# Kernel optimization log

Measured on AMD Instinct MI355X. Metric: run time of the kernel, lower is better.

Reference implementation:

```python
import jax, jax.numpy as jnp
import numpy as np

B, N, DIM, H, DH = 8, 1024, 512, 8, 64
INNER = H * DH  # 512
G = DH // 4     # SE(3) groups of size 4 per head


def setup_inputs() -> dict:
    key = jax.random.key(0)
    ks = jax.random.split(key, 6)
    x = jax.random.normal(ks[0], (B, N, DIM), jnp.float32)
    rotations = jax.random.normal(ks[1], (B, N, 3, 3), jnp.float32)
    translations = jax.random.normal(ks[2], (B, N, 3), jnp.float32)
    # JaxLinear init: trunc-normal std = 1/sqrt(fan_in), zero bias
    w_qkv = jax.random.normal(ks[3], (DIM, 3 * INNER), jnp.float32) * (1.0 / np.sqrt(DIM))
    b_qkv = jnp.zeros((3 * INNER,), jnp.float32)
    w_out = jax.random.normal(ks[4], (INNER, DIM), jnp.float32) * (1.0 / np.sqrt(INNER))
    b_out = jnp.zeros((DIM,), jnp.float32)
    return {"x": x, "rotations": rotations, "translations": translations,
            "w_qkv": w_qkv, "b_qkv": b_qkv, "w_out": w_out, "b_out": b_out}


def _apply_pose(P, t, transpose):
    # P: [B,N,4,4]; t: [B,H,N,DH] -> reshape to groups of 4 and rotate each group
    tg = t.reshape(B, H, N, G, 4)
    sub = 'bnji,bhncj->bhnci' if transpose else 'bnij,bhncj->bhnci'
    return jnp.einsum(sub, P, tg).reshape(B, H, N, DH)


def reference(x, rotations, translations, w_qkv, b_qkv, w_out, b_out):
    scale = DH ** -0.5
    qkv = x @ w_qkv + b_qkv                      # [B,N,3*INNER]
    q, k, v = jnp.split(qkv, 3, axis=-1)
    to_heads = lambda t: t.reshape(B, N, H, DH).transpose(0, 2, 1, 3)  # b n (h d) -> b h n d
    q, k, v = to_heads(q), to_heads(k), to_heads(v)

    # SE(3) pose matrices
    eye4 = jnp.eye(4, dtype=x.dtype)
    Rt = jnp.swapaxes(rotations, -1, -2)
    t_inv = -jnp.einsum('bnij,bnj->bni', Rt, translations)
    P_qinv = (jnp.broadcast_to(eye4, (B, N, 4, 4))
              .at[..., :3, :3].set(Rt)
              .at[..., :3, 3].set(t_inv))       # inverted query poses
    P_kv = (jnp.broadcast_to(eye4, (B, N, 4, 4))
            .at[..., :3, :3].set(rotations)
            .at[..., :3, 3].set(translations))  # key/value poses

    # per-token rotation of q/k/v (q uses P_qinv^T per original einsum)
    q = _apply_pose(P_qinv, q, transpose=True)
    k = _apply_pose(P_kv, k, transpose=False)
    v = _apply_pose(P_kv, v, transpose=False)   # v_transform=True

    attn = jax.nn.softmax(jnp.einsum('bhqd,bhkd->bhqk', q, k) * scale, axis=-1)
    out = jnp.einsum('bhqk,bhkd->bhqd', attn, v)
    out = _apply_pose(P_qinv, out, transpose=False)  # inverse transform on output

    out = out.transpose(0, 2, 1, 3).reshape(B, N, INNER)  # b h n d -> b n (h d)
    return out @ w_out + b_out
```

## Files before the change

kernel.cpp:

```cpp
#include <hip/hip_runtime.h>
#include <math.h>

#define BSZ   8
#define NSEQ  1024
#define DIM   512
#define NH    8
#define DH    64
#define INNER 512
#define NTOK  (BSZ*NSEQ)
#define QKVN  (3*INNER)

typedef __bf16 bf16x8 __attribute__((ext_vector_type(8)));
typedef float  f32x4  __attribute__((ext_vector_type(4)));

#define QSCL (0.125f * 1.44269504088896f)

#define ATTN_P_OFF 49152
#define ATTN_LDS   67584

static __device__ __forceinline__ ushort f2bf(float f) {
    union { float f; unsigned u; } v; v.f = f;
    unsigned r = (v.u + 0x7FFFu + ((v.u >> 16) & 1u)) >> 16;
    return (ushort)r;
}
static __device__ __forceinline__ float bf2f(ushort u) {
    union { unsigned u; float f; } v; v.u = ((unsigned)u) << 16;
    return v.f;
}
static __device__ __forceinline__ void split2(float x, ushort& h, ushort& l) {
    h = f2bf(x);
    l = f2bf(x - bf2f(h));
}
static __device__ __forceinline__ void async16(const void* g, void* l) {
    __builtin_amdgcn_global_load_lds(
        (const __attribute__((address_space(1))) unsigned int*)g,
        (__attribute__((address_space(3))) unsigned int*)l, 16, 0, 0);
}

__global__ __launch_bounds__(256) void split_cvt_kernel(
    const float* __restrict__ in, ushort* __restrict__ oh, ushort* __restrict__ ol)
{
    const int i = blockIdx.x * 256 + threadIdx.x;
    float4 v = ((const float4*)in)[i];
    ushort4 h, l;
    split2(v.x, h.x, l.x); split2(v.y, h.y, l.y);
    split2(v.z, h.z, l.z); split2(v.w, h.w, l.w);
    ((ushort4*)oh)[i] = h;
    ((ushort4*)ol)[i] = l;
}

__global__ __launch_bounds__(256) void tconv_kernel(
    const float* __restrict__ in, ushort* __restrict__ outh, int K, int F)
{
    __shared__ float tile[32][33];
    const int bx = blockIdx.x;
    const int by = blockIdx.y;
    const int lx = threadIdx.x & 31, ly = threadIdx.x >> 5;
#pragma unroll
    for (int u = 0; u < 4; u++) {
        const int k = by*32 + ly + u*8;
        tile[ly + u*8][lx] = in[(size_t)k*F + bx*32 + lx];
    }
    __syncthreads();
#pragma unroll
    for (int u = 0; u < 4; u++) {
        const int f = bx*32 + ly + u*8;
        outh[(size_t)f*K + by*32 + lx] = f2bf(tile[lx][ly + u*8]);
    }
}

__global__ __launch_bounds__(256) void qkv_gemm_split(
    const ushort* __restrict__ Agh, const ushort* __restrict__ Bgh,
    const ushort* __restrict__ Bgl,
    const float* __restrict__ bias, const float* __restrict__ rot,
    const float* __restrict__ trans,
    ushort* __restrict__ qb, ushort* __restrict__ kb, ushort* __restrict__ vt)
{
    extern __shared__ __align__(16) char smem[];

    const int tid  = threadIdx.x;
    const int lane = tid & 63;
    const int w    = tid >> 6;
    const int c    = lane & 15;
    const int quad = lane >> 4;
    const int wr   = w >> 1, wc = w & 1;
    const int tn   = blockIdx.x;
    const int tf   = blockIdx.y;

    f32x4 acc[4][4] = {};

    const ushort* wp = (w == 0) ? Agh : (w == 1) ? Bgh : Bgl;
    const ushort* wbase = wp + (size_t)((w == 0 ? tf : tn)*128 + c)*DIM + quad*8;
    const int lbase = w * 8192;

    auto stage = [&](int k0, int buf) {
        if (w < 3) {
#pragma unroll
            for (int g = 0; g < 8; g++)
                async16(wbase + (size_t)g*16*DIM + k0,
                        smem + buf*24576 + lbase + g*1024);
        }
    };

    stage(0, 0);

    for (int ch = 0; ch < 16; ch++) {
        const int cur = ch & 1, nxt = cur ^ 1;
        if (ch < 15) {
            stage((ch+1)*32, nxt);
            __asm__ volatile("s_waitcnt vmcnt(8)\n\ts_barrier" ::: "memory");
        } else {
            __asm__ volatile("s_waitcnt vmcnt(0)\n\ts_barrier" ::: "memory");
        }

        const char* B = smem + cur*24576;
        bf16x8 fa[4], fbh[4], fbl[4];
#pragma unroll
        for (int i = 0; i < 4; i++)
            fa[i] = *(const bf16x8*)(B + (wr*4 + i)*1024 + lane*16);
#pragma unroll
        for (int j = 0; j < 4; j++) {
            fbh[j] = *(const bf16x8*)(B +  8192 + (wc*4 + j)*1024 + lane*16);
            fbl[j] = *(const bf16x8*)(B + 16384 + (wc*4 + j)*1024 + lane*16);
        }
#pragma unroll
        for (int i = 0; i < 4; i++)
#pragma unroll
            for (int j = 0; j < 4; j++) {
                acc[i][j] = __builtin_amdgcn_mfma_f32_16x16x32_bf16(
                    fa[i], fbh[j], acc[i][j], 0, 0, 0);
                acc[i][j] = __builtin_amdgcn_mfma_f32_16x16x32_bf16(
                    fa[i], fbl[j], acc[i][j], 0, 0, 0);
            }
        __asm__ volatile("s_waitcnt lgkmcnt(0)\n\ts_barrier" ::: "memory");
    }

    const int sec = tf >> 2;

#pragma unroll
    for (int j = 0; j < 4; j++) {
        const int tc = tn*128 + wc*64 + j*16 + c;
        const int bb = tc >> 10, n = tc & 1023;
        const float* R = rot   + (size_t)(bb*NSEQ + n)*9;
        const float* T = trans + (size_t)(bb*NSEQ + n)*3;
        const float R0=R[0],R1=R[1],R2=R[2],R3=R[3],R4=R[4],R5=R[5],R6=R[6],R7=R[7],R8=R[8];
        const float T0=T[0],T1=T[1],T2=T[2];
        float ti0 = 0.f, ti1 = 0.f, ti2 = 0.f;
        if (sec == 0) {
            ti0 = -(R0*T0 + R3*T1 + R6*T2);
            ti1 = -(R1*T0 + R4*T1 + R7*T2);
            ti2 = -(R2*T0 + R5*T1 + R8*T2);
        }
#pragma unroll
        for (int i = 0; i < 4; i++) {
            const int fr = tf*128 + wr*64 + i*16 + quad*4;
            const int fl = fr & 511;
            const int h  = fl >> 6, d = fl & 63;
            float4 bv = *(const float4*)(bias + fr);
            const float g0 = acc[i][j][0] + bv.x;
            const float g1 = acc[i][j][1] + bv.y;
            const float g2 = acc[i][j][2] + bv.z;
            const float g3 = acc[i][j][3] + bv.w;
            if (sec == 0) {
                float o0 = (R0*g0 + R1*g1 + R2*g2) * QSCL;
                float o1 = (R3*g0 + R4*g1 + R5*g2) * QSCL;
                float o2 = (R6*g0 + R7*g1 + R8*g2) * QSCL;
                float o3 = (ti0*g0 + ti1*g1 + ti2*g2 + g3) * QSCL;
                ushort4 ov = { f2bf(o0), f2bf(o1), f2bf(o2), f2bf(o3) };
                *(ushort4*)(qb + ((size_t)((bb*NH + h)*NSEQ + n))*DH + d) = ov;
            } else {
                float o0 = R0*g0 + R1*g1 + R2*g2 + T0*g3;
                float o1 = R3*g0 + R4*g1 + R5*g2 + T1*g3;
                float o2 = R6*g0 + R7*g1 + R8*g2 + T2*g3;
                float o3 = g3;
                if (sec == 1) {
                    ushort4 ov = { f2bf(o0), f2bf(o1), f2bf(o2), f2bf(o3) };
                    *(ushort4*)(kb + ((size_t)((bb*NH + h)*NSEQ + n))*DH + d) = ov;
                } else {
                    ushort* vtb = vt + ((size_t)(bb*NH + h)*DH + d)*NSEQ + n;
                    vtb[0*NSEQ] = f2bf(o0);
                    vtb[1*NSEQ] = f2bf(o1);
                    vtb[2*NSEQ] = f2bf(o2);
                    vtb[3*NSEQ] = f2bf(o3);
                }
            }
        }
    }
}

__global__ __launch_bounds__(256) void attn_mfma_kernel(
    const ushort* __restrict__ qb, const ushort* __restrict__ kb,
    const ushort* __restrict__ vt, const float* __restrict__ rot,
    const float* __restrict__ trans, ushort* __restrict__ om)
{
    extern __shared__ __align__(16) char smem[];

    const int tid  = threadIdx.x;
    const int lane = tid & 63;
    const int w    = tid >> 6;
    const int c    = lane & 15;
    const int quad = lane >> 4;

    const int qt = blockIdx.x;
    const int bh = blockIdx.y;
    const int bb = bh >> 3, h = bh & 7;

    const ushort* Q = qb + (size_t)bh * NSEQ * DH;
    const ushort* K = kb + (size_t)bh * NSEQ * DH;
    const ushort* V = vt + (size_t)bh * DH * NSEQ;

    bf16x8 qf[2][2];
#pragma unroll
    for (int m = 0; m < 2; m++) {
        const ushort* qrow = Q + (size_t)(qt*128 + w*32 + m*16 + c)*DH + quad*8;
        qf[m][0] = *(const bf16x8*)(qrow);
        qf[m][1] = *(const bf16x8*)(qrow + 32);
    }

    f32x4 Oacc[2][4] = {};
    float lsum[2][4] = {};

    auto stage = [&](int kt, int buf) {
#pragma unroll
        for (int u = 0; u < 2; u++) {
            const int seg = w + u*4;
            const int nt = seg >> 1, hh = seg & 1;
            const ushort* g = K + (size_t)(kt*64 + nt*16 + c)*DH + hh*32 + quad*8;
            async16(g, smem + buf*16384 + seg*1024);
        }
#pragma unroll
        for (int u = 0; u < 2; u++) {
            const int s2 = w + u*4;
            const int nt = s2 >> 1, kc = s2 & 1;
            const ushort* g = V + (size_t)(nt*16 + c)*NSEQ + kt*64 + kc*32 + quad*8;
            async16(g, smem + buf*16384 + 8192 + s2*1024);
        }
    };

    stage(0, 0);
    stage(1, 1);

    for (int kt = 0; kt < 16; kt++) {
        const int cur = kt % 3;
        if (kt < 15) {
            __asm__ volatile("s_waitcnt vmcnt(4)\n\ts_barrier" ::: "memory");
        } else {
            __asm__ volatile("s_waitcnt vmcnt(0)\n\ts_barrier" ::: "memory");
        }
        if (kt < 14) stage(kt + 2, (kt + 2) % 3);

        const char* Kb = smem + cur*16384;
        const char* Vb = smem + cur*16384 + 8192;

        f32x4 s[2][4];
#pragma unroll
        for (int nt = 0; nt < 4; nt++) {
            bf16x8 k0 = *(const bf16x8*)(Kb + (nt*2+0)*1024 + lane*16);
            bf16x8 k1 = *(const bf16x8*)(Kb + (nt*2+1)*1024 + lane*16);
#pragma unroll
            for (int m = 0; m < 2; m++) {
                f32x4 a = {0.f, 0.f, 0.f, 0.f};
                a = __builtin_amdgcn_mfma_f32_16x16x32_bf16(qf[m][0], k0, a, 0, 0, 0);
                a = __builtin_amdgcn_mfma_f32_16x16x32_bf16(qf[m][1], k1, a, 0, 0, 0);
                s[m][nt] = a;
            }
        }

#pragma unroll
        for (int m = 0; m < 2; m++) {
            ushort (*Psw)[72] = (ushort (*)[72])(smem + ATTN_P_OFF + (w*2+m)*2304);
#pragma unroll
            for (int nt = 0; nt < 4; nt++)
#pragma unroll
                for (int r = 0; r < 4; r++) {
                    const float p = exp2f(s[m][nt][r]);
                    lsum[m][r] += p;
                    Psw[quad*4 + r][nt*16 + c] = (ushort)__builtin_bit_cast(
                        unsigned short, (__bf16)p);
                }
        }
        __asm__ volatile("s_waitcnt lgkmcnt(0)" ::: "memory");

#pragma unroll
        for (int kc = 0; kc < 2; kc++) {
            bf16x8 vfr[4];
#pragma unroll
            for (int nt = 0; nt < 4; nt++)
                vfr[nt] = *(const bf16x8*)(Vb + (nt*2+kc)*1024 + lane*16);
#pragma unroll
            for (int m = 0; m < 2; m++) {
                ushort (*Psw)[72] = (ushort (*)[72])(smem + ATTN_P_OFF + (w*2+m)*2304);
                bf16x8 a = *(const bf16x8*)&Psw[c][kc*32 + quad*8];
#pragma unroll
                for (int nt = 0; nt < 4; nt++)
                    Oacc[m][nt] = __builtin_amdgcn_mfma_f32_16x16x32_bf16(
                        a, vfr[nt], Oacc[m][nt], 0, 0, 0);
            }
        }
    }

#pragma unroll
    for (int mk = 1; mk < 16; mk <<= 1)
#pragma unroll
        for (int m = 0; m < 2; m++)
#pragma unroll
            for (int r = 0; r < 4; r++)
                lsum[m][r] += __shfl_xor(lsum[m][r], mk);

    __syncthreads();
    float (*Osh)[68] = (float (*)[68])smem;
    {
        float inv[2][4];
#pragma unroll
        for (int m = 0; m < 2; m++)
#pragma unroll
            for (int r = 0; r < 4; r++) inv[m][r] = 1.f / lsum[m][r];
#pragma unroll
        for (int m = 0; m < 2; m++)
#pragma unroll
            for (int nt = 0; nt < 4; nt++)
#pragma unroll
                for (int r = 0; r < 4; r++)
                    Osh[w*32 + m*16 + quad*4 + r][nt*16 + c] =
                        Oacc[m][nt][r] * inv[m][r];
    }
    __syncthreads();

#pragma unroll
    for (int u = 0; u < 8; u++) {
        const int t   = tid + u*256;
        const int row = t >> 4;
        const int g   = t & 15;
        const int n   = qt*128 + row;
        const float o0 = Osh[row][g*4+0], o1 = Osh[row][g*4+1];
        const float o2 = Osh[row][g*4+2], o3 = Osh[row][g*4+3];
        const float* R = rot   + (size_t)(bb*NSEQ + n)*9;
        const float* T = trans + (size_t)(bb*NSEQ + n)*3;
        const float ti0 = -(R[0]*T[0] + R[3]*T[1] + R[6]*T[2]);
        const float ti1 = -(R[1]*T[0] + R[4]*T[1] + R[7]*T[2]);
        const float ti2 = -(R[2]*T[0] + R[5]*T[1] + R[8]*T[2]);
        const float p0 = R[0]*o0 + R[3]*o1 + R[6]*o2 + ti0*o3;
        const float p1 = R[1]*o0 + R[4]*o1 + R[7]*o2 + ti1*o3;
        const float p2 = R[2]*o0 + R[5]*o1 + R[8]*o2 + ti2*o3;
        const float p3 = o3;
        ushort4 hv = { f2bf(p0), f2bf(p1), f2bf(p2), f2bf(p3) };
        *(ushort4*)(om + (size_t)(bb*NSEQ + n)*INNER + h*DH + g*4) = hv;
    }
}

__global__ __launch_bounds__(256) void out_gemm_mfma(
    const ushort* __restrict__ Ag, const ushort* __restrict__ Bg,
    const float* __restrict__ bias, float* __restrict__ out)
{
    extern __shared__ __align__(16) char smem[];

    const int tid  = threadIdx.x;
    const int lane = tid & 63;
    const int w    = tid >> 6;
    const int c    = lane & 15;
    const int quad = lane >> 4;
    const int wr   = w >> 1, wc = w & 1;
    const int tn   = blockIdx.x;
    const int tf   = blockIdx.y;

    f32x4 acc[4][4] = {};

    const int part = w >> 1;
    const int g0   = (w & 1) * 4;
    const ushort* src = (part == 0) ? Ag : Bg;
    const ushort* wbase = src + (size_t)((part == 0 ? tf : tn)*128 + g0*16 + c)*INNER
                          + quad*8;

    auto stage = [&](int k0, int buf) {
#pragma unroll
        for (int g = 0; g < 4; g++)
            async16(wbase + (size_t)g*16*INNER + k0,
                    smem + buf*16384 + part*8192 + (g0 + g)*1024);
    };

    stage(0, 0);
    stage(32, 1);
    stage(64, 2);

    for (int ch = 0; ch < 16; ch++) {
        const int cur = ch & 3;
        if (ch < 14) {
            __asm__ volatile("s_waitcnt vmcnt(8)\n\ts_barrier" ::: "memory");
        } else if (ch == 14) {
            __asm__ volatile("s_waitcnt vmcnt(4)\n\ts_barrier" ::: "memory");
        } else {
            __asm__ volatile("s_waitcnt vmcnt(0)\n\ts_barrier" ::: "memory");
        }
        if (ch < 13) stage((ch+3)*32, (ch+3) & 3);

        const char* B = smem + cur*16384;
        bf16x8 fa[4], fb[4];
#pragma unroll
        for (int i = 0; i < 4; i++)
            fa[i] = *(const bf16x8*)(B + (wr*4 + i)*1024 + lane*16);
#pragma unroll
        for (int j = 0; j < 4; j++)
            fb[j] = *(const bf16x8*)(B + 8192 + (wc*4 + j)*1024 + lane*16);
#pragma unroll
        for (int i = 0; i < 4; i++)
#pragma unroll
            for (int j = 0; j < 4; j++)
                acc[i][j] = __builtin_amdgcn_mfma_f32_16x16x32_bf16(
                    fa[i], fb[j], acc[i][j], 0, 0, 0);
    }

#pragma unroll
    for (int j = 0; j < 4; j++) {
        const int tc = tn*128 + wc*64 + j*16 + c;
#pragma unroll
        for (int i = 0; i < 4; i++) {
            const int fr = tf*128 + wr*64 + i*16 + quad*4;
            float4 bv = *(const float4*)(bias + fr);
            float4 ov = { acc[i][j][0] + bv.x, acc[i][j][1] + bv.y,
                          acc[i][j][2] + bv.z, acc[i][j][3] + bv.w };
            *(float4*)(out + (size_t)tc*DIM + fr) = ov;
        }
    }
}

extern "C" void kernel_launch(void* const* d_in, const int* in_sizes, int n_in,
                              void* d_out, int out_size, void* d_ws, size_t ws_size,
                              hipStream_t stream) {
    (void)in_sizes; (void)n_in; (void)out_size; (void)ws_size;
    const float* x     = (const float*)d_in[0];
    const float* rot   = (const float*)d_in[1];
    const float* trans = (const float*)d_in[2];
    const float* w_qkv = (const float*)d_in[3];
    const float* b_qkv = (const float*)d_in[4];
    const float* w_out = (const float*)d_in[5];
    const float* b_out = (const float*)d_in[6];
    float* out = (float*)d_out;

    const size_t HB = (size_t)BSZ*NH*NSEQ*DH;
    ushort* qb   = (ushort*)d_ws;
    ushort* kb   = qb   + HB;
    ushort* vt   = kb   + HB;
    ushort* woTh = vt   + HB;
    ushort* wqTh = woTh + (size_t)DIM*INNER;
    ushort* xh   = wqTh + (size_t)QKVN*DIM;
    ushort* xl   = xh   + HB;
    ushort* om   = xh;

    static int s_attr_done = 0;
    if (!s_attr_done) {
        (void)hipFuncSetAttribute((const void*)attn_mfma_kernel,
            hipFuncAttributeMaxDynamicSharedMemorySize, ATTN_LDS);
        (void)hipFuncSetAttribute((const void*)out_gemm_mfma,
            hipFuncAttributeMaxDynamicSharedMemorySize, 65536);
        s_attr_done = 1;
    }

    split_cvt_kernel<<<dim3(NTOK*DIM/1024), 256, 0, stream>>>(x, xh, xl);
    tconv_kernel<<<dim3(QKVN/32, DIM/32), 256, 0, stream>>>(w_qkv, wqTh, DIM, QKVN);
    tconv_kernel<<<dim3(DIM/32, INNER/32), 256, 0, stream>>>(w_out, woTh, INNER, DIM);

    qkv_gemm_split<<<dim3(NTOK/128, QKVN/128), 256, 49152, stream>>>(
        wqTh, xh, xl, b_qkv, rot, trans, qb, kb, vt);
    attn_mfma_kernel<<<dim3(NSEQ/128, BSZ*NH), 256, ATTN_LDS, stream>>>(
        qb, kb, vt, rot, trans, om);
    out_gemm_mfma<<<dim3(NTOK/128, DIM/128), 256, 65536, stream>>>(
        woTh, om, b_out, out);
}
```

Measured before the change: 178.9 us.

## Use single-pass fp16 QKV GEMM instead of split bf16 and fuse prep kernels

The QKV projection switches from a split-bf16 scheme (x as hi+lo bf16, two MFMAs per tile) to plain fp16 inputs with one f16 MFMA per tile. That halves the MFMA count, shrinks LDS staging, and removes the xl buffer. The three preprocessing kernels (x convert, two weight transposes) are merged into one launch. fp16 has less range but more mantissa than bf16, so accuracy should stay close for these normalized inputs, though it loses the extra precision of the split.

```diff
diff --git a/kernel.cpp b/kernel.cpp
--- a/kernel.cpp
+++ b/kernel.cpp
@@ -10,8 +10,9 @@
 #define NTOK  (BSZ*NSEQ)
 #define QKVN  (3*INNER)
 
-typedef __bf16 bf16x8 __attribute__((ext_vector_type(8)));
-typedef float  f32x4  __attribute__((ext_vector_type(4)));
+typedef __bf16   bf16x8 __attribute__((ext_vector_type(8)));
+typedef _Float16 f16x8  __attribute__((ext_vector_type(8)));
+typedef float    f32x4  __attribute__((ext_vector_type(4)));
 
 #define QSCL (0.125f * 1.44269504088896f)
 
@@ -23,13 +24,9 @@
     unsigned r = (v.u + 0x7FFFu + ((v.u >> 16) & 1u)) >> 16;
     return (ushort)r;
 }
-static __device__ __forceinline__ float bf2f(ushort u) {
-    union { unsigned u; float f; } v; v.u = ((unsigned)u) << 16;
-    return v.f;
-}
-static __device__ __forceinline__ void split2(float x, ushort& h, ushort& l) {
-    h = f2bf(x);
-    l = f2bf(x - bf2f(h));
+static __device__ __forceinline__ ushort f2h(float f) {
+    _Float16 h = (_Float16)f;
+    return __builtin_bit_cast(unsigned short, h);
 }
 static __device__ __forceinline__ void async16(const void* g, void* l) {
     __builtin_amdgcn_global_load_lds(
@@ -37,24 +34,30 @@
         (__attribute__((address_space(3))) unsigned int*)l, 16, 0, 0);
 }
 
-__global__ __launch_bounds__(256) void split_cvt_kernel(
-    const float* __restrict__ in, ushort* __restrict__ oh, ushort* __restrict__ ol)
+__global__ __launch_bounds__(256) void prep_kernel(
+    const float* __restrict__ x,  ushort* __restrict__ xf,
+    const float* __restrict__ wq, ushort* __restrict__ wqT,
+    const float* __restrict__ wo, ushort* __restrict__ woT)
 {
-    const int i = blockIdx.x * 256 + threadIdx.x;
-    float4 v = ((const float4*)in)[i];
-    ushort4 h, l;
-    split2(v.x, h.x, l.x); split2(v.y, h.y, l.y);
-    split2(v.z, h.z, l.z); split2(v.w, h.w, l.w);
-    ((ushort4*)oh)[i] = h;
-    ((ushort4*)ol)[i] = l;
-}
-
-__global__ __launch_bounds__(256) void tconv_kernel(
-    const float* __restrict__ in, ushort* __restrict__ outh, int K, int F)
-{
+    const int bid = blockIdx.x;
+    if (bid < 4096) {
+        const int i = bid*256 + threadIdx.x;
+        float4 v = ((const float4*)x)[i];
+        ushort4 h = { f2h(v.x), f2h(v.y), f2h(v.z), f2h(v.w) };
+        ((ushort4*)xf)[i] = h;
+        return;
+    }
     __shared__ float tile[32][33];
-    const int bx = blockIdx.x;
-    const int by = blockIdx.y;
+    int K, F, bx, by; const float* in; ushort* outp; int is_q;
+    if (bid < 4096 + 768) {
+        const int id = bid - 4096;
+        bx = id % 48; by = id / 48;
+        K = DIM; F = QKVN; in = wq; outp = wqT; is_q = 1;
+    } else {
+        const int id = bid - 4864;
+        bx = id % 16; by = id / 16;
+        K = INNER; F = DIM; in = wo; outp = woT; is_q = 0;
+    }
     const int lx = threadIdx.x & 31, ly = threadIdx.x >> 5;
 #pragma unroll
     for (int u = 0; u < 4; u++) {
@@ -65,13 +68,14 @@
 #pragma unroll
     for (int u = 0; u < 4; u++) {
         const int f = bx*32 + ly + u*8;
-        outh[(size_t)f*K + by*32 + lx] = f2bf(tile[lx][ly + u*8]);
-    }
-}
-
-__global__ __launch_bounds__(256) void qkv_gemm_split(
-    const ushort* __restrict__ Agh, const ushort* __restrict__ Bgh,
-    const ushort* __restrict__ Bgl,
+        const float v = tile[lx][ly + u*8];
+        outp[(size_t)f*K + by*32 + lx] = is_q ? f2h(v) : f2bf(v);
+    }
+}
+
+__global__ __launch_bounds__(256) void qkv_gemm_f16(
+    const ushort* __restrict__ Ag,
+    const ushort* __restrict__ Bg,
     const float* __restrict__ bias, const float* __restrict__ rot,
     const float* __restrict__ trans,
     ushort* __restrict__ qb, ushort* __restrict__ kb, ushort* __restrict__ vt)
@@ -89,17 +93,17 @@
 
     f32x4 acc[4][4] = {};
 
-    const ushort* wp = (w == 0) ? Agh : (w == 1) ? Bgh : Bgl;
-    const ushort* wbase = wp + (size_t)((w == 0 ? tf : tn)*128 + c)*DIM + quad*8;
-    const int lbase = w * 8192;
+    const int part = w >> 1;
+    const int g0   = (w & 1) * 4;
+    const ushort* src = (part == 0) ? Ag : Bg;
+    const ushort* wbase = src + (size_t)((part == 0 ? tf : tn)*128 + g0*16 + c)*DIM
+                          + quad*8;
 
     auto stage = [&](int k0, int buf) {
-        if (w < 3) {
-#pragma unroll
-            for (int g = 0; g < 8; g++)
-                async16(wbase + (size_t)g*16*DIM + k0,
-                        smem + buf*24576 + lbase + g*1024);
-        }
+#pragma unroll
+        for (int g = 0; g < 4; g++)
+            async16(wbase + (size_t)g*16*DIM + k0,
+                    smem + buf*16384 + part*8192 + (g0 + g)*1024);
     };
 
     stage(0, 0);
@@ -108,30 +112,25 @@
         const int cur = ch & 1, nxt = cur ^ 1;
         if (ch < 15) {
             stage((ch+1)*32, nxt);
-            __asm__ volatile("s_waitcnt vmcnt(8)\n\ts_barrier" ::: "memory");
+            __asm__ volatile("s_waitcnt vmcnt(4)\n\ts_barrier" ::: "memory");
         } else {
             __asm__ volatile("s_waitcnt vmcnt(0)\n\ts_barrier" ::: "memory");
         }
 
-        const char* B = smem + cur*24576;
-        bf16x8 fa[4], fbh[4], fbl[4];
+        const char* B = smem + cur*16384;
+        f16x8 fa[4], fb[4];
 #pragma unroll
         for (int i = 0; i < 4; i++)
-            fa[i] = *(const bf16x8*)(B + (wr*4 + i)*1024 + lane*16);
-#pragma unroll
-        for (int j = 0; j < 4; j++) {
-            fbh[j] = *(const bf16x8*)(B +  8192 + (wc*4 + j)*1024 + lane*16);
-            fbl[j] = *(const bf16x8*)(B + 16384 + (wc*4 + j)*1024 + lane*16);
-        }
+            fa[i] = *(const f16x8*)(B + (wr*4 + i)*1024 + lane*16);
+#pragma unroll
+        for (int j = 0; j < 4; j++)
+            fb[j] = *(const f16x8*)(B + 8192 + (wc*4 + j)*1024 + lane*16);
 #pragma unroll
         for (int i = 0; i < 4; i++)
 #pragma unroll
-            for (int j = 0; j < 4; j++) {
-                acc[i][j] = __builtin_amdgcn_mfma_f32_16x16x32_bf16(
-                    fa[i], fbh[j], acc[i][j], 0, 0, 0);
-                acc[i][j] = __builtin_amdgcn_mfma_f32_16x16x32_bf16(
-                    fa[i], fbl[j], acc[i][j], 0, 0, 0);
-            }
+            for (int j = 0; j < 4; j++)
+                acc[i][j] = __builtin_amdgcn_mfma_f32_16x16x32_f16(
+                    fa[i], fb[j], acc[i][j], 0, 0, 0);
         __asm__ volatile("s_waitcnt lgkmcnt(0)\n\ts_barrier" ::: "memory");
     }
 
@@ -157,22 +156,22 @@
             const int fl = fr & 511;
             const int h  = fl >> 6, d = fl & 63;
             float4 bv = *(const float4*)(bias + fr);
-            const float g0 = acc[i][j][0] + bv.x;
-            const float g1 = acc[i][j][1] + bv.y;
-            const float g2 = acc[i][j][2] + bv.z;
-            const float g3 = acc[i][j][3] + bv.w;
+            const float g0v = acc[i][j][0] + bv.x;
+            const float g1v = acc[i][j][1] + bv.y;
+            const float g2v = acc[i][j][2] + bv.z;
+            const float g3v = acc[i][j][3] + bv.w;
             if (sec == 0) {
-                float o0 = (R0*g0 + R1*g1 + R2*g2) * QSCL;
-                float o1 = (R3*g0 + R4*g1 + R5*g2) * QSCL;
-                float o2 = (R6*g0 + R7*g1 + R8*g2) * QSCL;
-                float o3 = (ti0*g0 + ti1*g1 + ti2*g2 + g3) * QSCL;
+                float o0 = (R0*g0v + R1*g1v + R2*g2v) * QSCL;
+                float o1 = (R3*g0v + R4*g1v + R5*g2v) * QSCL;
+                float o2 = (R6*g0v + R7*g1v + R8*g2v) * QSCL;
+                float o3 = (ti0*g0v + ti1*g1v + ti2*g2v + g3v) * QSCL;
                 ushort4 ov = { f2bf(o0), f2bf(o1), f2bf(o2), f2bf(o3) };
                 *(ushort4*)(qb + ((size_t)((bb*NH + h)*NSEQ + n))*DH + d) = ov;
             } else {
-                float o0 = R0*g0 + R1*g1 + R2*g2 + T0*g3;
-                float o1 = R3*g0 + R4*g1 + R5*g2 + T1*g3;
-                float o2 = R6*g0 + R7*g1 + R8*g2 + T2*g3;
-                float o3 = g3;
+                float o0 = R0*g0v + R1*g1v + R2*g2v + T0*g3v;
+                float o1 = R3*g0v + R4*g1v + R5*g2v + T1*g3v;
+                float o2 = R6*g0v + R7*g1v + R8*g2v + T2*g3v;
+                float o3 = g3v;
                 if (sec == 1) {
                     ushort4 ov = { f2bf(o0), f2bf(o1), f2bf(o2), f2bf(o3) };
                     *(ushort4*)(kb + ((size_t)((bb*NH + h)*NSEQ + n))*DH + d) = ov;
@@ -442,9 +441,8 @@
     ushort* vt   = kb   + HB;
     ushort* woTh = vt   + HB;
     ushort* wqTh = woTh + (size_t)DIM*INNER;
-    ushort* xh   = wqTh + (size_t)QKVN*DIM;
-    ushort* xl   = xh   + HB;
-    ushort* om   = xh;
+    ushort* xf   = wqTh + (size_t)QKVN*DIM;
+    ushort* om   = xf;
 
     static int s_attr_done = 0;
     if (!s_attr_done) {
@@ -455,12 +453,11 @@
         s_attr_done = 1;
     }
 
-    split_cvt_kernel<<<dim3(NTOK*DIM/1024), 256, 0, stream>>>(x, xh, xl);
-    tconv_kernel<<<dim3(QKVN/32, DIM/32), 256, 0, stream>>>(w_qkv, wqTh, DIM, QKVN);
-    tconv_kernel<<<dim3(DIM/32, INNER/32), 256, 0, stream>>>(w_out, woTh, INNER, DIM);
-
-    qkv_gemm_split<<<dim3(NTOK/128, QKVN/128), 256, 49152, stream>>>(
-        wqTh, xh, xl, b_qkv, rot, trans, qb, kb, vt);
+    prep_kernel<<<dim3(5120), 256, 0, stream>>>(
+        x, xf, w_qkv, wqTh, w_out, woTh);
+
+    qkv_gemm_f16<<<dim3(NTOK/128, QKVN/128), 256, 32768, stream>>>(
+        wqTh, xf, b_qkv, rot, trans, qb, kb, vt);
     attn_mfma_kernel<<<dim3(NSEQ/128, BSZ*NH), 256, ATTN_LDS, stream>>>(
         qb, kb, vt, rot, trans, om);
     out_gemm_mfma<<<dim3(NTOK/128, DIM/128), 256, 65536, stream>>>(
```

Result: faster. 164.7 us (-7.9%).
